# Kernel optimization log

Measured on AMD Instinct MI355X. Metric: run time of the kernel, lower is better.

## Reference

```python
import jax, jax.numpy as jnp
import numpy as np

DIM = 512
HEADS = 8
DHEAD = DIM // 8          # 64
INNER = HEADS * DHEAD     # 512
M_LANDMARKS = 256
PINV_ITERS = 6
KSZ = 33                  # residual depthwise conv kernel (default)


def setup_inputs() -> dict:
    key = jax.random.key(0)
    ks = jax.random.split(key, 5)
    B, N = 1, 16384
    s = DIM ** -0.5
    return {
        "x": jax.random.normal(ks[0], (B, N, DIM), jnp.float32),
        "norm_w": jnp.ones((DIM,), jnp.float32),
        "norm_b": jnp.zeros((DIM,), jnp.float32),
        "w_qkv": jax.random.normal(ks[1], (3 * INNER, DIM), jnp.float32) * s,   # Linear(dim, 3*inner, bias=False)
        "w_out": jax.random.normal(ks[2], (DIM, INNER), jnp.float32) * s,        # Linear(inner, dim)
        "b_out": jnp.zeros((DIM,), jnp.float32),
        "conv_w": jax.random.normal(ks[3], (HEADS, 1, KSZ, 1), jnp.float32) * 0.1,  # depthwise Conv2d(h,h,(33,1),groups=h)
    }


def _layernorm(x, w, b, eps=1e-5):
    mu = x.mean(-1, keepdims=True)
    var = ((x - mu) ** 2).mean(-1, keepdims=True)
    return (x - mu) * jax.lax.rsqrt(var + eps) * w + b


def _moore_penrose_pinv(a, iters):
    # a: [B, H, m, m]; matches lucidrains moore_penrose_iter_pinv (global max over col/row sums)
    abs_a = jnp.abs(a)
    col = abs_a.sum(-1).max()
    row = abs_a.sum(-2).max()
    z = jnp.swapaxes(a, -1, -2) / (col * row)
    I = jnp.eye(a.shape[-1], dtype=a.dtype)
    for _ in range(iters):
        az = a @ z
        z = 0.25 * z @ (13 * I - az @ (15 * I - az @ (7 * I - az)))
    return z


def _nystrom_attention(h, w_qkv, w_out, b_out, conv_w):
    B, N, _ = h.shape
    qkv = h @ w_qkv.T                          # [B, N, 3*inner]
    q, k, v = jnp.split(qkv, 3, axis=-1)

    def heads(t):
        return t.reshape(B, N, HEADS, DHEAD).transpose(0, 2, 1, 3)  # [B, H, N, d]
    q = heads(q) * (DHEAD ** -0.5)
    k = heads(k)
    v = heads(v)

    # landmark pooling: mean over contiguous groups of size l = N / m
    l = N // M_LANDMARKS
    q_l = q.reshape(B, HEADS, M_LANDMARKS, l, DHEAD).mean(3)   # [B, H, m, d]
    k_l = k.reshape(B, HEADS, M_LANDMARKS, l, DHEAD).mean(3)

    attn1 = jax.nn.softmax(jnp.einsum('bhnd,bhmd->bhnm', q, k_l), axis=-1)      # [B,H,N,m]
    attn2 = jax.nn.softmax(jnp.einsum('bhid,bhjd->bhij', q_l, k_l), axis=-1)    # [B,H,m,m]
    attn3 = jax.nn.softmax(jnp.einsum('bhmd,bhnd->bhmn', q_l, k), axis=-1)      # [B,H,m,N]

    attn2_inv = _moore_penrose_pinv(attn2, PINV_ITERS)
    out = attn1 @ (attn2_inv @ (attn3 @ v))                                     # [B,H,N,d]

    # residual depthwise conv along sequence dim (kernel 33x1, groups=HEADS, no bias)
    conv = jax.lax.conv_general_dilated(
        v, conv_w, window_strides=(1, 1),
        padding=((KSZ // 2, KSZ // 2), (0, 0)),
        dimension_numbers=('NCHW', 'OIHW', 'NCHW'),
        feature_group_count=HEADS)
    out = out + conv

    out = out.transpose(0, 2, 1, 3).reshape(B, N, INNER)
    return out @ w_out.T + b_out


def reference(x, norm_w, norm_b, w_qkv, w_out, b_out, conv_w):
    h = _layernorm(x, norm_w, norm_b)
    return x + _nystrom_attention(h, w_qkv, w_out, b_out, conv_w)
```

## Files before the change

kernel.cpp:

```cpp
#include <hip/hip_runtime.h>
#include <hip/hip_bf16.h>


typedef __attribute__((ext_vector_type(8))) short bf16x8;
typedef __attribute__((ext_vector_type(4))) float f32x4;

#define MFMA16(A, B, C) __builtin_amdgcn_mfma_f32_16x16x32_bf16(A, B, C, 0, 0, 0)
#define GLD16(g, l) __builtin_amdgcn_global_load_lds( \
    (const __attribute__((address_space(1))) void*)(g), \
    (__attribute__((address_space(3))) void*)(l), 16, 0, 0)

static __device__ __forceinline__ unsigned short f2b(float f) {
  __hip_bfloat16 h = __float2bfloat16(f);
  return *reinterpret_cast<unsigned short*>(&h);
}
static __device__ __forceinline__ float b2f(unsigned short u) {
  return __uint_as_float(((unsigned)u) << 16);
}

#define FMA16(ACC, AV, BV) do { \
  ACC[0][0] += AV.x*BV.x; ACC[0][1] += AV.x*BV.y; ACC[0][2] += AV.x*BV.z; ACC[0][3] += AV.x*BV.w; \
  ACC[1][0] += AV.y*BV.x; ACC[1][1] += AV.y*BV.y; ACC[1][2] += AV.y*BV.z; ACC[1][3] += AV.y*BV.w; \
  ACC[2][0] += AV.z*BV.x; ACC[2][1] += AV.z*BV.y; ACC[2][2] += AV.z*BV.z; ACC[2][3] += AV.z*BV.w; \
  ACC[3][0] += AV.w*BV.x; ACC[3][1] += AV.w*BV.y; ACC[3][2] += AV.w*BV.z; ACC[3][3] += AV.w*BV.w; \
} while (0)

__global__ __launch_bounds__(128) void k_ln(const float* __restrict__ x,
    const float* __restrict__ w, const float* __restrict__ b, unsigned short* __restrict__ h) {
  const int row = blockIdx.x;
  const int t = threadIdx.x;
  const float4 xv = ((const float4*)(x + (size_t)row * 512))[t];
  float s  = xv.x + xv.y + xv.z + xv.w;
  float sq = xv.x*xv.x + xv.y*xv.y + xv.z*xv.z + xv.w*xv.w;
  #pragma unroll
  for (int o = 32; o > 0; o >>= 1) {
    s  += __shfl_down(s, o, 64);
    sq += __shfl_down(sq, o, 64);
  }
  __shared__ float ls[2], lq[2];
  if ((t & 63) == 0) { ls[t >> 6] = s; lq[t >> 6] = sq; }
  __syncthreads();
  s = ls[0] + ls[1]; sq = lq[0] + lq[1];
  const float mean = s * (1.0f / 512.0f);
  const float var  = sq * (1.0f / 512.0f) - mean * mean;
  const float rstd = rsqrtf(var + 1e-5f);
  const float4 wv = ((const float4*)w)[t];
  const float4 bv = ((const float4*)b)[t];
  ushort4 hv;
  hv.x = f2b((xv.x - mean) * rstd * wv.x + bv.x);
  hv.y = f2b((xv.y - mean) * rstd * wv.y + bv.y);
  hv.z = f2b((xv.z - mean) * rstd * wv.z + bv.z);
  hv.w = f2b((xv.w - mean) * rstd * wv.w + bv.w);
  ((ushort4*)(h + (size_t)row * 512))[t] = hv;
}

__global__ __launch_bounds__(256) void k_cvt(const float* __restrict__ src,
    unsigned short* __restrict__ dst, int n4) {
  const int i = blockIdx.x * 256 + threadIdx.x;
  if (i < n4) {
    const float4 f = ((const float4*)src)[i];
    ushort4 u;
    u.x = f2b(f.x); u.y = f2b(f.y); u.z = f2b(f.z); u.w = f2b(f.w);
    ((ushort4*)dst)[i] = u;
  }
}

__global__ __launch_bounds__(256) void k_qkv_mfma(const unsigned short* __restrict__ A,
    const unsigned short* __restrict__ B,
    unsigned short* __restrict__ qb, unsigned short* __restrict__ kb,
    unsigned short* __restrict__ vb) {
  __shared__ unsigned short As[128 * 32];
  __shared__ unsigned short Bs[128 * 32];
  const int t = threadIdx.x;
  const int lane = t & 63, w = t >> 6;
  const int quad = lane >> 4, l15 = lane & 15;
  const int wm = (w >> 1) * 64, wn = (w & 1) * 64;
  const int m0 = blockIdx.y * 128, n0 = blockIdx.x * 128;
  f32x4 acc[4][4];
  #pragma unroll
  for (int i = 0; i < 4; ++i)
    #pragma unroll
    for (int j = 0; j < 4; ++j) acc[i][j] = (f32x4){0.f, 0.f, 0.f, 0.f};
  for (int k0 = 0; k0 < 512; k0 += 32) {
    __syncthreads();
    #pragma unroll
    for (int c = 0; c < 2; ++c) {
      const int slot = c * 256 + t;
      const int row = slot >> 2, seg = slot & 3;
      GLD16(A + (size_t)(m0 + row) * 512 + k0 + seg * 8, As + slot * 8);
      GLD16(B + (size_t)(n0 + row) * 512 + k0 + seg * 8, Bs + slot * 8);
    }
    __syncthreads();
    bf16x8 a[4], b[4];
    #pragma unroll
    for (int i = 0; i < 4; ++i)
      a[i] = *(const bf16x8*)(As + (wm + i * 16 + l15) * 32 + quad * 8);
    #pragma unroll
    for (int j = 0; j < 4; ++j)
      b[j] = *(const bf16x8*)(Bs + (wn + j * 16 + l15) * 32 + quad * 8);
    #pragma unroll
    for (int i = 0; i < 4; ++i)
      #pragma unroll
      for (int j = 0; j < 4; ++j)
        acc[i][j] = MFMA16(a[i], b[j], acc[i][j]);
  }
  const int part = n0 >> 9;
  #pragma unroll
  for (int i = 0; i < 4; ++i)
    #pragma unroll
    for (int j = 0; j < 4; ++j)
      #pragma unroll
      for (int r = 0; r < 4; ++r) {
        const int row = m0 + wm + i * 16 + quad * 4 + r;
        const int col = n0 + wn + j * 16 + l15;
        const int rem = col & 511;
        const int hd = rem >> 6, dd = rem & 63;
        const size_t idx = ((size_t)hd * 16384 + row) * 64 + dd;
        const float val = acc[i][j][r];
        if (part == 0)      qb[idx] = f2b(val * 0.125f);
        else if (part == 1) kb[idx] = f2b(val);
        else                vb[idx] = f2b(val);
      }
}

__global__ __launch_bounds__(256) void k_tr(const unsigned short* __restrict__ v,
    unsigned short* __restrict__ vt) {
  __shared__ unsigned short T[64][72];
  const int t = threadIdx.x;
  const int n0 = blockIdx.x * 64, h = blockIdx.y;
  const int n = t >> 2, sg = (t & 3) * 16;
  const unsigned short* p = v + ((size_t)(h * 16384 + n0 + n)) * 64 + sg;
  #pragma unroll
  for (int i = 0; i < 16; i += 4) {
    const ushort4 u = *(const ushort4*)(p + i);
    T[sg + i + 0][n] = u.x; T[sg + i + 1][n] = u.y;
    T[sg + i + 2][n] = u.z; T[sg + i + 3][n] = u.w;
  }
  __syncthreads();
  const int d = t >> 2, so = (t & 3) * 16;
  unsigned short* q = vt + ((size_t)(h * 64 + d)) * 16384 + n0 + so;
  #pragma unroll
  for (int i = 0; i < 16; i += 4) {
    ushort4 u;
    u.x = T[d][so + i]; u.y = T[d][so + i + 1];
    u.z = T[d][so + i + 2]; u.w = T[d][so + i + 3];
    *(ushort4*)(q + i) = u;
  }
}

__global__ __launch_bounds__(256) void k_landmark(const unsigned short* __restrict__ qb,
    const unsigned short* __restrict__ kb, float* __restrict__ qlf,
    unsigned short* __restrict__ qlb, float* __restrict__ klf,
    unsigned short* __restrict__ klb) {
  const int t = threadIdx.x, d = t & 63, grp = t >> 6;
  const int m = blockIdx.x, h = blockIdx.y;
  const unsigned short* src = blockIdx.z ? kb : qb;
  const unsigned short* p = src + ((size_t)h * 16384 + m * 64 + grp * 16) * 64 + d;
  float s = 0.f;
  #pragma unroll
  for (int i = 0; i < 16; ++i) s += b2f(p[(size_t)i * 64]);
  __shared__ float red[4][64];
  red[grp][d] = s;
  __syncthreads();
  if (t < 64) {
    float v = (red[0][d] + red[1][d]) + (red[2][d] + red[3][d]);
    v *= (1.0f / 64.0f);
    const size_t oi = ((size_t)h * 256 + m) * 64 + d;
    if (blockIdx.z == 0) { qlf[oi] = v; qlb[oi] = f2b(v); }
    else                 { klf[oi] = v; klb[oi] = f2b(v); }
  }
}

__global__ __launch_bounds__(256) void k_attn2(const float* __restrict__ ql,
    const float* __restrict__ kl, float* __restrict__ a2, unsigned short* __restrict__ a2b) {
  const int i = blockIdx.x, h = blockIdx.y, j = threadIdx.x;
  __shared__ float qrow[64];
  __shared__ float wred[4];
  __shared__ float wsum[4];
  if (j < 64) qrow[j] = ql[((size_t)h * 256 + i) * 64 + j];
  __syncthreads();
  const float* kr = kl + ((size_t)h * 256 + j) * 64;
  float s = 0.f;
  #pragma unroll 8
  for (int d = 0; d < 64; ++d) s += qrow[d] * kr[d];
  float mx = s;
  #pragma unroll
  for (int o2 = 32; o2 > 0; o2 >>= 1) mx = fmaxf(mx, __shfl_xor(mx, o2, 64));
  if ((j & 63) == 0) wred[j >> 6] = mx;
  __syncthreads();
  mx = fmaxf(fmaxf(wred[0], wred[1]), fmaxf(wred[2], wred[3]));
  const float e = __expf(s - mx);
  float sm = e;
  #pragma unroll
  for (int o2 = 32; o2 > 0; o2 >>= 1) sm += __shfl_xor(sm, o2, 64);
  if ((j & 63) == 0) wsum[j >> 6] = sm;
  __syncthreads();
  sm = wsum[0] + wsum[1] + wsum[2] + wsum[3];
  const float v = e / sm;
  const size_t idx = ((size_t)h * 256 + i) * 256 + j;
  a2[idx] = v;
  a2b[idx] = f2b(v);
}

__global__ __launch_bounds__(256) void k_colsum(const float* __restrict__ a2,
    float* __restrict__ cm) {
  const int h = blockIdx.x, j = threadIdx.x;
  const float* p = a2 + (size_t)h * 65536 + j;
  float s = 0.f;
  for (int i = 0; i < 256; ++i) s += p[(size_t)i * 256];
  float mx = s;
  #pragma unroll
  for (int o2 = 32; o2 > 0; o2 >>= 1) mx = fmaxf(mx, __shfl_xor(mx, o2, 64));
  __shared__ float wred[4];
  if ((j & 63) == 0) wred[j >> 6] = mx;
  __syncthreads();
  if (j == 0) cm[h] = fmaxf(fmaxf(wred[0], wred[1]), fmaxf(wred[2], wred[3]));
}

__global__ __launch_bounds__(256) void k_z0(const float* __restrict__ a2,
    const float* __restrict__ cm, unsigned short* __restrict__ z0b,
    unsigned short* __restrict__ z0t) {
  __shared__ float T[64][65];
  const int bi = blockIdx.x, bj = blockIdx.y, h = blockIdx.z;
  const int t = threadIdx.x;
  const int r = t >> 2, cseg = (t & 3) * 16;
  float g = cm[0];
  #pragma unroll
  for (int c = 1; c < 8; ++c) g = fmaxf(g, cm[c]);
  const float inv = 1.0f / g;
  const float* p = a2 + ((size_t)h * 256 + bj * 64 + r) * 256 + bi * 64 + cseg;
  unsigned short* qt = z0t + ((size_t)h * 256 + bj * 64 + r) * 256 + bi * 64 + cseg;
  #pragma unroll
  for (int i = 0; i < 16; i += 4) {
    const float4 f = *(const float4*)(p + i);
    T[cseg + i + 0][r] = f.x; T[cseg + i + 1][r] = f.y;
    T[cseg + i + 2][r] = f.z; T[cseg + i + 3][r] = f.w;
    ushort4 u;
    u.x = f2b(f.x * inv); u.y = f2b(f.y * inv);
    u.z = f2b(f.z * inv); u.w = f2b(f.w * inv);
    *(ushort4*)(qt + i) = u;
  }
  __syncthreads();
  unsigned short* qb_ = z0b + ((size_t)h * 256 + bi * 64 + r) * 256 + bj * 64 + cseg;
  #pragma unroll
  for (int i = 0; i < 16; i += 4) {
    ushort4 u;
    u.x = f2b(T[r][cseg + i] * inv);     u.y = f2b(T[r][cseg + i + 1] * inv);
    u.z = f2b(T[r][cseg + i + 2] * inv); u.w = f2b(T[r][cseg + i + 3] * inv);
    *(ushort4*)(qb_ + i) = u;
  }
}

__global__ __launch_bounds__(256) void k_pgemm(const unsigned short* __restrict__ A,
    const unsigned short* __restrict__ Bt, unsigned short* __restrict__ Cn,
    unsigned short* __restrict__ Ct, float* __restrict__ Cf,
    float alpha, float sdiag, int use_diag) {
  __shared__ unsigned short As[64 * 128];
  __shared__ unsigned short Bs[64 * 128];
  const int t = threadIdx.x;
  const int lane = t & 63, w = t >> 6;
  const int quad = lane >> 4, l15 = lane & 15;
  const int bn = blockIdx.x, bm = blockIdx.y, h = blockIdx.z;
  const size_t hs = (size_t)h * 65536;
  const unsigned short* Ap = A + hs + (size_t)(bm * 64) * 256;
  const unsigned short* Bp = Bt + hs + (size_t)(bn * 64) * 256;
  f32x4 acc[4];
  #pragma unroll
  for (int j = 0; j < 4; ++j) acc[j] = (f32x4){0.f, 0.f, 0.f, 0.f};
  for (int kh = 0; kh < 2; ++kh) {
    __syncthreads();
    #pragma unroll
    for (int c = 0; c < 4; ++c) {
      const int slot = c * 256 + t;
      const int row = slot >> 4, pc = slot & 15;
      const int lc = pc ^ (row & 7);
      GLD16(Ap + (size_t)row * 256 + kh * 128 + lc * 8, As + slot * 8);
      GLD16(Bp + (size_t)row * 256 + kh * 128 + lc * 8, Bs + slot * 8);
    }
    __syncthreads();
    #pragma unroll
    for (int kc = 0; kc < 4; ++kc) {
      const int arow = w * 16 + l15;
      const bf16x8 a = *(const bf16x8*)(As + arow * 128 + ((kc * 4 + quad) ^ (arow & 7)) * 8);
      #pragma unroll
      for (int j = 0; j < 4; ++j) {
        const int brow = j * 16 + l15;
        const bf16x8 b = *(const bf16x8*)(Bs + brow * 128 + ((kc * 4 + quad) ^ (brow & 7)) * 8);
        acc[j] = MFMA16(a, b, acc[j]);
      }
    }
  }
  const int row0 = bm * 64 + w * 16 + quad * 4;
  #pragma unroll
  for (int j = 0; j < 4; ++j) {
    const int col = bn * 64 + j * 16 + l15;
    float v[4];
    #pragma unroll
    for (int r = 0; r < 4; ++r) v[r] = acc[j][r] * alpha;
    if (Cn) {
      #pragma unroll
      for (int r = 0; r < 4; ++r) Cn[hs + (size_t)(row0 + r) * 256 + col] = f2b(v[r]);
    }
    if (Cf) {
      #pragma unroll
      for (int r = 0; r < 4; ++r) Cf[hs + (size_t)(row0 + r) * 256 + col] = v[r];
    }
    ushort4 u;
    float tv[4];
    #pragma unroll
    for (int r = 0; r < 4; ++r)
      tv[r] = use_diag ? ((col == row0 + r ? sdiag : 0.f) - v[r]) : v[r];
    u.x = f2b(tv[0]); u.y = f2b(tv[1]); u.z = f2b(tv[2]); u.w = f2b(tv[3]);
    *(ushort4*)(Ct + hs + (size_t)col * 256 + row0) = u;
  }
}

__global__ __launch_bounds__(256) void k_gemm256(const float* __restrict__ A,
    const float* __restrict__ B, float* __restrict__ C,
    int lda, int ldb, int ldc,
    unsigned long long sA, unsigned long long sB, unsigned long long sC,
    float alpha, float sdiag, int use_diag,
    const float* __restrict__ rs, unsigned long long sRS) {
  A += (size_t)blockIdx.z * sA;
  B += (size_t)blockIdx.z * sB;
  C += (size_t)blockIdx.z * sC;
  if (rs) rs += (size_t)blockIdx.z * sRS;
  __shared__ float As[16][68];
  __shared__ float Bs[16][68];
  const int t = threadIdx.x, tx = t & 15, ty = t >> 4;
  const int bn = blockIdx.x, bm = blockIdx.y;
  const int lr = t >> 2, lk = (t & 3) << 2;
  const int bkr = t >> 4, bnc = (t & 15) << 2;
  float acc[4][4] = {{0.f}};
  for (int k0 = 0; k0 < 256; k0 += 16) {
    float4 a4 = *(const float4*)(A + (size_t)(bm * 64 + lr) * lda + k0 + lk);
    float4 b4 = *(const float4*)(B + (size_t)(k0 + bkr) * ldb + bn * 64 + bnc);
    if (use_diag) {
      const int kg = k0 + bkr, ngb = bn * 64 + bnc;
      b4.x = (kg == ngb + 0 ? sdiag : 0.f) - b4.x;
      b4.y = (kg == ngb + 1 ? sdiag : 0.f) - b4.y;
      b4.z = (kg == ngb + 2 ? sdiag : 0.f) - b4.z;
      b4.w = (kg == ngb + 3 ? sdiag : 0.f) - b4.w;
    }
    if (rs) {
      const float rv = 1.0f / rs[k0 + bkr];
      b4.x *= rv; b4.y *= rv; b4.z *= rv; b4.w *= rv;
    }
    __syncthreads();
    As[lk+0][lr] = a4.x; As[lk+1][lr] = a4.y; As[lk+2][lr] = a4.z; As[lk+3][lr] = a4.w;
    *(float4*)&Bs[bkr][bnc] = b4;
    __syncthreads();
    #pragma unroll
    for (int kq = 0; kq < 16; ++kq) {
      const float4 av = *(const float4*)&As[kq][ty << 2];
      const float4 bv = *(const float4*)&Bs[kq][tx << 2];
      FMA16(acc, av, bv);
    }
  }
  #pragma unroll
  for (int ii = 0; ii < 4; ++ii)
    #pragma unroll
    for (int jj = 0; jj < 4; ++jj)
      C[(size_t)(bm * 64 + (ty << 2) + ii) * ldc + bn * 64 + (tx << 2) + jj] =
          alpha * acc[ii][jj];
}

__global__ __launch_bounds__(256) void k_trD(const float* __restrict__ D,
    unsigned short* __restrict__ dt) {
  __shared__ float T[64][65];
  const int t = threadIdx.x;
  const int mc = blockIdx.x, h = blockIdx.y;
  const int m = t >> 2, sg = (t & 3) * 16;
  const float* p = D + ((size_t)(h * 256 + mc * 64 + m)) * 64 + sg;
  #pragma unroll
  for (int i = 0; i < 16; i += 4) {
    const float4 f = *(const float4*)(p + i);
    T[sg + i + 0][m] = f.x; T[sg + i + 1][m] = f.y;
    T[sg + i + 2][m] = f.z; T[sg + i + 3][m] = f.w;
  }
  __syncthreads();
  const int d = t >> 2, so = (t & 3) * 16;
  unsigned short* q = dt + ((size_t)(h * 64 + d)) * 256 + mc * 64 + so;
  #pragma unroll
  for (int i = 0; i < 16; i += 4) {
    ushort4 u;
    u.x = f2b(T[d][so + i]);     u.y = f2b(T[d][so + i + 1]);
    u.z = f2b(T[d][so + i + 2]); u.w = f2b(T[d][so + i + 3]);
    *(ushort4*)(q + i) = u;
  }
}

__global__ __launch_bounds__(256) void k_w3_mfma(const unsigned short* __restrict__ qlb,
    const unsigned short* __restrict__ kb, const unsigned short* __restrict__ vt,
    float* __restrict__ W, float* __restrict__ lsum) {
  __shared__ unsigned short QLs[64 * 64];
  __shared__ unsigned short Ks [64 * 64];
  __shared__ unsigned short Vts[64 * 64];
  __shared__ unsigned short Ps [64 * 64];
  const int t = threadIdx.x;
  const int lane = t & 63, w = t >> 6;
  const int quad = lane >> 4, l15 = lane & 15;
  const int kc = blockIdx.x, mt = blockIdx.y, h = blockIdx.z;
  #pragma unroll
  for (int c = 0; c < 2; ++c) {
    const int slot = c * 256 + t;
    const int row = slot >> 3, pc = slot & 7, lc = pc ^ (row & 7);
    GLD16(qlb + ((size_t)(h * 256 + mt * 64 + row)) * 64 + lc * 8, QLs + slot * 8);
  }
  __syncthreads();
  const int arow = w * 16 + l15;
  const bf16x8 aq0 = *(const bf16x8*)(QLs + arow * 64 + ((quad    ) ^ (arow & 7)) * 8);
  const bf16x8 aq1 = *(const bf16x8*)(QLs + arow * 64 + ((quad + 4) ^ (arow & 7)) * 8);
  f32x4 wacc[4];
  #pragma unroll
  for (int dt = 0; dt < 4; ++dt) wacc[dt] = (f32x4){0.f, 0.f, 0.f, 0.f};
  float lacc[4] = {0.f, 0.f, 0.f, 0.f};
  for (int ss = 0; ss < 16; ++ss) {
    const int n0 = kc * 1024 + ss * 64;
    __syncthreads();
    #pragma unroll
    for (int c = 0; c < 2; ++c) {
      const int slot = c * 256 + t;
      const int row = slot >> 3, pc = slot & 7, lc = pc ^ (row & 7);
      GLD16(kb + ((size_t)(h * 16384 + n0 + row)) * 64 + lc * 8, Ks + slot * 8);
      GLD16(vt + ((size_t)(h * 64 + row)) * 16384 + n0 + lc * 8, Vts + slot * 8);
    }
    __syncthreads();
    f32x4 s[4];
    #pragma unroll
    for (int j = 0; j < 4; ++j) {
      s[j] = (f32x4){0.f, 0.f, 0.f, 0.f};
      const int brow = j * 16 + l15;
      const bf16x8 b0 = *(const bf16x8*)(Ks + brow * 64 + ((quad    ) ^ (brow & 7)) * 8);
      const bf16x8 b1 = *(const bf16x8*)(Ks + brow * 64 + ((quad + 4) ^ (brow & 7)) * 8);
      s[j] = MFMA16(aq0, b0, s[j]);
      s[j] = MFMA16(aq1, b1, s[j]);
    }
    #pragma unroll
    for (int j = 0; j < 4; ++j)
      #pragma unroll
      for (int r = 0; r < 4; ++r) {
        const float e = __expf(s[j][r]);
        lacc[r] += e;
        const int prow = w * 16 + quad * 4 + r, pcol = j * 16 + l15;
        Ps[prow * 64 + (((pcol >> 3) ^ (prow & 7)) << 3) + (pcol & 7)] = f2b(e);
      }
    __syncthreads();
    const bf16x8 ap0 = *(const bf16x8*)(Ps + arow * 64 + ((quad    ) ^ (arow & 7)) * 8);
    const bf16x8 ap1 = *(const bf16x8*)(Ps + arow * 64 + ((quad + 4) ^ (arow & 7)) * 8);
    #pragma unroll
    for (int dt = 0; dt < 4; ++dt) {
      const int brow = dt * 16 + l15;
      const bf16x8 b0 = *(const bf16x8*)(Vts + brow * 64 + ((quad    ) ^ (brow & 7)) * 8);
      const bf16x8 b1 = *(const bf16x8*)(Vts + brow * 64 + ((quad + 4) ^ (brow & 7)) * 8);
      wacc[dt] = MFMA16(ap0, b0, wacc[dt]);
      wacc[dt] = MFMA16(ap1, b1, wacc[dt]);
    }
  }
  #pragma unroll
  for (int dt = 0; dt < 4; ++dt)
    #pragma unroll
    for (int r = 0; r < 4; ++r)
      atomicAdd(&W[((size_t)(h * 256 + mt * 64 + w * 16 + quad * 4 + r)) * 64 + dt * 16 + l15],
                wacc[dt][r]);
  #pragma unroll
  for (int r = 0; r < 4; ++r) {
    #pragma unroll
    for (int msk = 1; msk < 16; msk <<= 1) lacc[r] += __shfl_xor(lacc[r], msk, 64);
    if (l15 == 0)
      atomicAdd(&lsum[h * 256 + mt * 64 + w * 16 + quad * 4 + r], lacc[r]);
  }
}
// ... 28 lines not shown
    const int n = t >> 2;
    const int gb = (t & 3) * 24;
    #pragma unroll
    for (int i = 0; i < 24; ++i) {
      const int g = gb + i;
      const int j = g - n;
      const int src = n0 - 16 + g;
      const float val = (j >= 0 && j <= 32 && src >= 0 && src < 16384) ? Wsm[j] : 0.f;
      Wb[n * 96 + (((g >> 3) ^ (n & 3)) << 3) + (g & 7)] = f2b(val);
    }
  }
  __syncthreads();
  f32x4 cacc[4];
  #pragma unroll
  for (int dt = 0; dt < 4; ++dt) cacc[dt] = (f32x4){0.f, 0.f, 0.f, 0.f};
  #pragma unroll
  for (int kcc = 0; kcc < 3; ++kcc) {
    const bf16x8 a = *(const bf16x8*)(Wb + arow * 96 + (((kcc * 4 + quad) ^ (arow & 3)) << 3));
    int off = n0 - 16 + kcc * 32 + quad * 8;
    off = off < 0 ? 0 : (off > 16376 ? 16376 : off);
    #pragma unroll
    for (int dt = 0; dt < 4; ++dt) {
      const bf16x8 b = *(const bf16x8*)(vt + ((size_t)(h * 64 + dt * 16 + l15)) * 16384 + off);
      cacc[dt] = MFMA16(a, b, cacc[dt]);
    }
  }
  f32x4 oacc[4];
  #pragma unroll
  for (int dt = 0; dt < 4; ++dt) oacc[dt] = (f32x4){0.f, 0.f, 0.f, 0.f};
  float lacc[4] = {0.f, 0.f, 0.f, 0.f};
  for (int mc = 0; mc < 4; ++mc) {
    const int m0 = mc * 64;
    __syncthreads();
    #pragma unroll
    for (int c = 0; c < 2; ++c) {
      const int slot = c * 256 + t;
      const int row = slot >> 3, pc = slot & 7, lc = pc ^ (row & 7);
      GLD16(klb + ((size_t)(h * 256 + m0 + row)) * 64 + lc * 8, Ks + slot * 8);
      GLD16(dtb + ((size_t)(h * 64 + row)) * 256 + m0 + lc * 8, Ds + slot * 8);
    }
    __syncthreads();
    f32x4 s[4];
    #pragma unroll
    for (int j = 0; j < 4; ++j) {
      s[j] = (f32x4){0.f, 0.f, 0.f, 0.f};
      const int brow = j * 16 + l15;
      const bf16x8 b0 = *(const bf16x8*)(Ks + brow * 64 + ((quad    ) ^ (brow & 7)) * 8);
      const bf16x8 b1 = *(const bf16x8*)(Ks + brow * 64 + ((quad + 4) ^ (brow & 7)) * 8);
      s[j] = MFMA16(aq0, b0, s[j]);
      s[j] = MFMA16(aq1, b1, s[j]);
    }
    #pragma unroll
    for (int j = 0; j < 4; ++j)
      #pragma unroll
      for (int r = 0; r < 4; ++r) {
        const float e = __expf(s[j][r]);
        lacc[r] += e;
        const int prow = w * 16 + quad * 4 + r, pcol = j * 16 + l15;
        Ps[prow * 64 + (((pcol >> 3) ^ (prow & 7)) << 3) + (pcol & 7)] = f2b(e);
      }
    __syncthreads();
    const bf16x8 ap0 = *(const bf16x8*)(Ps + arow * 64 + ((quad    ) ^ (arow & 7)) * 8);
    const bf16x8 ap1 = *(const bf16x8*)(Ps + arow * 64 + ((quad + 4) ^ (arow & 7)) * 8);
    #pragma unroll
    for (int dt = 0; dt < 4; ++dt) {
      const int brow = dt * 16 + l15;
      const bf16x8 b0 = *(const bf16x8*)(Ds + brow * 64 + ((quad    ) ^ (brow & 7)) * 8);
      const bf16x8 b1 = *(const bf16x8*)(Ds + brow * 64 + ((quad + 4) ^ (brow & 7)) * 8);
      oacc[dt] = MFMA16(ap0, b0, oacc[dt]);
      oacc[dt] = MFMA16(ap1, b1, oacc[dt]);
    }
  }
  #pragma unroll
  for (int r = 0; r < 4; ++r)
    #pragma unroll
    for (int msk = 1; msk < 16; msk <<= 1) lacc[r] += __shfl_xor(lacc[r], msk, 64);
  #pragma unroll
  for (int dt = 0; dt < 4; ++dt)
    #pragma unroll
    for (int r = 0; r < 4; ++r) {
      const float val = oacc[dt][r] / lacc[r] + cacc[dt][r];
      o[((size_t)(n0 + w * 16 + quad * 4 + r)) * 512 + h * 64 + dt * 16 + l15] = f2b(val);
    }
}

__global__ __launch_bounds__(256) void k_out_mfma(const unsigned short* __restrict__ A,
    const unsigned short* __restrict__ B, const float* __restrict__ bias,
    const float* __restrict__ xres, float* __restrict__ out) {
  __shared__ unsigned short As[128 * 32];
  __shared__ unsigned short Bs[128 * 32];
  const int t = threadIdx.x;
  const int lane = t & 63, w = t >> 6;
  const int quad = lane >> 4, l15 = lane & 15;
  const int wm = (w >> 1) * 64, wn = (w & 1) * 64;
  const int m0 = blockIdx.y * 128, n0 = blockIdx.x * 128;
  f32x4 acc[4][4];
  #pragma unroll
  for (int i = 0; i < 4; ++i)
    #pragma unroll
    for (int j = 0; j < 4; ++j) acc[i][j] = (f32x4){0.f, 0.f, 0.f, 0.f};
  for (int k0 = 0; k0 < 512; k0 += 32) {
    __syncthreads();
    #pragma unroll
    for (int c = 0; c < 2; ++c) {
      const int slot = c * 256 + t;
      const int row = slot >> 2, seg = slot & 3;
      GLD16(A + (size_t)(m0 + row) * 512 + k0 + seg * 8, As + slot * 8);
      GLD16(B + (size_t)(n0 + row) * 512 + k0 + seg * 8, Bs + slot * 8);
    }
    __syncthreads();
    bf16x8 a[4], b[4];
    #pragma unroll
    for (int i = 0; i < 4; ++i)
      a[i] = *(const bf16x8*)(As + (wm + i * 16 + l15) * 32 + quad * 8);
    #pragma unroll
    for (int j = 0; j < 4; ++j)
      b[j] = *(const bf16x8*)(Bs + (wn + j * 16 + l15) * 32 + quad * 8);
    #pragma unroll
    for (int i = 0; i < 4; ++i)
      #pragma unroll
      for (int j = 0; j < 4; ++j)
        acc[i][j] = MFMA16(a[i], b[j], acc[i][j]);
  }
  #pragma unroll
  for (int i = 0; i < 4; ++i)
    #pragma unroll
    for (int j = 0; j < 4; ++j)
      #pragma unroll
      for (int r = 0; r < 4; ++r) {
        const int row = m0 + wm + i * 16 + quad * 4 + r;
        const int col = n0 + wn + j * 16 + l15;
        out[(size_t)row * 512 + col] = acc[i][j][r] + bias[col] + xres[(size_t)row * 512 + col];
      }
}

extern "C" void kernel_launch(void* const* d_in, const int* in_sizes, int n_in,
                              void* d_out, int out_size, void* d_ws, size_t ws_size,
                              hipStream_t stream) {
  const float* x      = (const float*)d_in[0];
  const float* norm_w = (const float*)d_in[1];
  const float* norm_b = (const float*)d_in[2];
  const float* w_qkv  = (const float*)d_in[3];
  const float* w_out  = (const float*)d_in[4];
  const float* b_out  = (const float*)d_in[5];
  const float* conv_w = (const float*)d_in[6];
  float* out = (float*)d_out;

  char* cur = (char*)d_ws;
  auto alloc = [&](size_t bytes) -> char* {
    char* p = cur;
    cur += (bytes + 255) & ~(size_t)255;
    return p;
  };
  const size_t NB = (size_t)16384 * 512;
  const size_t LM = (size_t)8 * 256 * 64;
  const size_t SQ = (size_t)8 * 256 * 256;

  unsigned short* h_b  = (unsigned short*)alloc(NB * 2);
  unsigned short* wq_b = (unsigned short*)alloc((size_t)1536 * 512 * 2);
  unsigned short* wo_b = (unsigned short*)alloc((size_t)512 * 512 * 2);
  unsigned short* qb   = (unsigned short*)alloc(NB * 2);
  unsigned short* kb   = (unsigned short*)alloc(NB * 2);
  unsigned short* vb   = (unsigned short*)alloc(NB * 2);
  unsigned short* vt   = (unsigned short*)alloc(NB * 2);
  float*          qlf  = (float*)alloc(LM * 4);
  float*          klf  = (float*)alloc(LM * 4);
  unsigned short* qlb  = (unsigned short*)alloc(LM * 2);
  unsigned short* klb  = (unsigned short*)alloc(LM * 2);
  float*          a2   = (float*)alloc(SQ * 4);
  unsigned short* a2b  = (unsigned short*)alloc(SQ * 2);
  unsigned short* z0b  = (unsigned short*)alloc(SQ * 2);
  unsigned short* z0t  = (unsigned short*)alloc(SQ * 2);
  unsigned short* Pn   = (unsigned short*)alloc(SQ * 2);
  unsigned short* Pt   = (unsigned short*)alloc(SQ * 2);
  unsigned short* Q1t  = (unsigned short*)alloc(SQ * 2);
  unsigned short* Q2t  = (unsigned short*)alloc(SQ * 2);
  unsigned short* zp0n = (unsigned short*)alloc(SQ * 2);
  unsigned short* zp0t = (unsigned short*)alloc(SQ * 2);
  unsigned short* zp1n = (unsigned short*)alloc(SQ * 2);
  unsigned short* zp1t = (unsigned short*)alloc(SQ * 2);
  float*          zf5  = (float*)alloc(SQ * 4);
  float*          zfin = (float*)alloc(SQ * 4);
  float*          Pp   = (float*)alloc(SQ * 4);
  float*          Q1   = (float*)alloc(SQ * 4);
  float*          Q2   = (float*)alloc(SQ * 4);
  float*          W    = (float*)alloc(LM * 4 + 2048 * 4);
  float*          lsum = W + LM;
  float*          D    = (float*)alloc(LM * 4);
  unsigned short* dtb  = (unsigned short*)alloc(LM * 2);
  float*          cm   = (float*)alloc(64 * 4);
  unsigned short* o_b  = (unsigned short*)alloc(NB * 2);

  hipMemsetAsync(W, 0, (LM + 2048) * sizeof(float), stream);
  k_ln<<<16384, 128, 0, stream>>>(x, norm_w, norm_b, h_b);
  k_cvt<<<768, 256, 0, stream>>>(w_qkv, wq_b, 196608);
  k_cvt<<<256, 256, 0, stream>>>(w_out, wo_b, 65536);
  k_qkv_mfma<<<dim3(12, 128), 256, 0, stream>>>(h_b, wq_b, qb, kb, vb);
  k_tr<<<dim3(256, 8), 256, 0, stream>>>(vb, vt);
  k_landmark<<<dim3(256, 8, 2), 256, 0, stream>>>(qb, kb, qlf, qlb, klf, klb);
  k_attn2<<<dim3(256, 8), 256, 0, stream>>>(qlf, klf, a2, a2b);
  k_colsum<<<8, 256, 0, stream>>>(a2, cm);
  k_z0<<<dim3(4, 4, 8), 256, 0, stream>>>(a2, cm, z0b, z0t);

  unsigned short* zan = z0b; unsigned short* zat = z0t;
  for (int it = 0; it < 5; ++it) {
    unsigned short* zbn = (it & 1) ? zp1n : zp0n;
    unsigned short* zbt = (it & 1) ? zp1t : zp0t;
    k_pgemm<<<dim3(4, 4, 8), 256, 0, stream>>>(a2b, zat, Pn, Pt, nullptr, 1.f, 7.f, 1);
    k_pgemm<<<dim3(4, 4, 8), 256, 0, stream>>>(Pn, Pt, nullptr, Q1t, nullptr, 1.f, 15.f, 1);
    k_pgemm<<<dim3(4, 4, 8), 256, 0, stream>>>(Pn, Q1t, nullptr, Q2t, nullptr, 1.f, 13.f, 1);
    k_pgemm<<<dim3(4, 4, 8), 256, 0, stream>>>(zan, Q2t, zbn, zbt,
        it == 4 ? zf5 : nullptr, 0.25f, 0.f, 0);
    zan = zbn; zat = zbt;
  }
  k_gemm256<<<dim3(4, 4, 8), 256, 0, stream>>>(a2, zf5, Pp, 256, 256, 256,
      65536ULL, 65536ULL, 65536ULL, 1.f, 0.f, 0, nullptr, 0ULL);
  k_gemm256<<<dim3(4, 4, 8), 256, 0, stream>>>(Pp, Pp, Q1, 256, 256, 256,
      65536ULL, 65536ULL, 65536ULL, 1.f, 7.f, 1, nullptr, 0ULL);
  k_gemm256<<<dim3(4, 4, 8), 256, 0, stream>>>(Pp, Q1, Q2, 256, 256, 256,
      65536ULL, 65536ULL, 65536ULL, 1.f, 15.f, 1, nullptr, 0ULL);
  k_gemm256<<<dim3(4, 4, 8), 256, 0, stream>>>(zf5, Q2, zfin, 256, 256, 256,
      65536ULL, 65536ULL, 65536ULL, 0.25f, 13.f, 1, nullptr, 0ULL);

  k_w3_mfma<<<dim3(16, 4, 8), 256, 0, stream>>>(qlb, kb, vt, W, lsum);
  k_gemm256<<<dim3(1, 4, 8), 256, 0, stream>>>(zfin, W, D, 256, 64, 64,
      65536ULL, 16384ULL, 16384ULL, 1.f, 0.f, 0, lsum, 256ULL);
  k_trD<<<dim3(4, 8), 256, 0, stream>>>(D, dtb);
  k_attn1_mfma<<<dim3(256, 8), 256, 0, stream>>>(qb, klb, dtb, vt, conv_w, o_b);
  k_out_mfma<<<dim3(4, 128), 256, 0, stream>>>(o_b, wo_b, b_out, x, out);
}
```

Baseline: 449.1 us.

## Rewrite QKV and output GEMMs with 256x256 tiles and triple-buffered LDS pipeline

Replaces the 128x128 single-buffered QKV and output-projection GEMMs with 512-thread 256x256 tile kernels. Global-to-LDS loads are triple-buffered using vmcnt waits and a single barrier per k-step, and MFMA issue is raised in priority with s_setprio. Block indices are swizzled for L2 locality. The fragment-friendly LDS layout removes bank conflicts. The larger tiles cut operand reloads, but the output GEMM now runs only 128 blocks, which may underfill the GPU's CUs, and 96KB of LDS per block limits occupancy.

```diff
diff --git a/kernel.cpp b/kernel.cpp
--- a/kernel.cpp
+++ b/kernel.cpp
@@ -65,62 +65,128 @@
   }
 }
 
-__global__ __launch_bounds__(256) void k_qkv_mfma(const unsigned short* __restrict__ A,
+__device__ __forceinline__ void stage_tile(const unsigned short* __restrict__ A,
+    const unsigned short* __restrict__ B, unsigned short* lds,
+    int m0, int n0, int k0, int tid) {
+  #pragma unroll
+  for (int c = 0; c < 2; ++c) {
+    const int s = c * 512 + tid;
+    const int grow = ((s >> 6) << 4) | (s & 15);
+    const int chunk = (s >> 4) & 3;
+    GLD16(A + (size_t)(m0 + grow) * 512 + k0 + chunk * 8, lds + s * 8);
+    GLD16(B + (size_t)(n0 + grow) * 512 + k0 + chunk * 8, lds + 8192 + s * 8);
+  }
+}
+
+__device__ __forceinline__ void compute_tile(const unsigned short* lds,
+    f32x4 (&acc)[8][4], int wr, int wc, int quad, int l15) {
+  bf16x8 a[8], b[4];
+  #pragma unroll
+  for (int i = 0; i < 8; ++i)
+    a[i] = *(const bf16x8*)(lds + (size_t)((wr * 8 + i) * 64 + quad * 16 + l15) * 8);
+  #pragma unroll
+  for (int j = 0; j < 4; ++j)
+    b[j] = *(const bf16x8*)(lds + 8192 + (size_t)((wc * 4 + j) * 64 + quad * 16 + l15) * 8);
+  __builtin_amdgcn_s_setprio(1);
+  #pragma unroll
+  for (int i = 0; i < 8; ++i)
+    #pragma unroll
+    for (int j = 0; j < 4; ++j)
+      acc[i][j] = MFMA16(a[i], b[j], acc[i][j]);
+  __builtin_amdgcn_s_setprio(0);
+}
+
+#define GEMM256_PIPELINE(Aptr, Bptr, M0, N0)                                 \
+  f32x4 acc[8][4];                                                           \
+  _Pragma("unroll")                                                          \
+  for (int i = 0; i < 8; ++i)                                                \
+    _Pragma("unroll")                                                        \
+    for (int j = 0; j < 4; ++j) acc[i][j] = (f32x4){0.f, 0.f, 0.f, 0.f};     \
+  stage_tile(Aptr, Bptr, lds, M0, N0, 0, tid);                               \
+  asm volatile("" ::: "memory");                                             \
+  stage_tile(Aptr, Bptr, lds + 16384, M0, N0, 32, tid);                      \
+  asm volatile("s_waitcnt vmcnt(4)" ::: "memory");                           \
+  __builtin_amdgcn_s_barrier();                                              \
+  {                                                                          \
+    int cb = 0, sb = 2;                                                      \
+    for (int t = 0; t < 14; ++t) {                                           \
+      stage_tile(Aptr, Bptr, lds + sb * 16384, M0, N0, (t + 2) * 32, tid);   \
+      compute_tile(lds + cb * 16384, acc, wr, wc, quad, l15);                \
+      asm volatile("s_waitcnt vmcnt(4)" ::: "memory");                       \
+      __builtin_amdgcn_s_barrier();                                          \
+      cb = (cb == 2) ? 0 : cb + 1;                                           \
+      sb = (sb == 2) ? 0 : sb + 1;                                           \
+    }                                                                        \
+    compute_tile(lds + cb * 16384, acc, wr, wc, quad, l15);                  \
+    cb = (cb == 2) ? 0 : cb + 1;                                             \
+    asm volatile("s_waitcnt vmcnt(0)" ::: "memory");                         \
+    __builtin_amdgcn_s_barrier();                                            \
+    compute_tile(lds + cb * 16384, acc, wr, wc, quad, l15);                  \
+  }
+
+__global__ __launch_bounds__(512, 2) void k_qkv2(const unsigned short* __restrict__ A,
     const unsigned short* __restrict__ B,
     unsigned short* __restrict__ qb, unsigned short* __restrict__ kb,
     unsigned short* __restrict__ vb) {
-  __shared__ unsigned short As[128 * 32];
-  __shared__ unsigned short Bs[128 * 32];
-  const int t = threadIdx.x;
-  const int lane = t & 63, w = t >> 6;
+  __shared__ unsigned short lds[49152];
+  const int tid = threadIdx.x;
+  const int lane = tid & 63, w = tid >> 6;
+  const int wr = w >> 2, wc = w & 3;
   const int quad = lane >> 4, l15 = lane & 15;
-  const int wm = (w >> 1) * 64, wn = (w & 1) * 64;
-  const int m0 = blockIdx.y * 128, n0 = blockIdx.x * 128;
-  f32x4 acc[4][4];
-  #pragma unroll
-  for (int i = 0; i < 4; ++i)
-    #pragma unroll
-    for (int j = 0; j < 4; ++j) acc[i][j] = (f32x4){0.f, 0.f, 0.f, 0.f};
-  for (int k0 = 0; k0 < 512; k0 += 32) {
-    __syncthreads();
-    #pragma unroll
-    for (int c = 0; c < 2; ++c) {
-      const int slot = c * 256 + t;
-      const int row = slot >> 2, seg = slot & 3;
-      GLD16(A + (size_t)(m0 + row) * 512 + k0 + seg * 8, As + slot * 8);
-      GLD16(B + (size_t)(n0 + row) * 512 + k0 + seg * 8, Bs + slot * 8);
-    }
-    __syncthreads();
-    bf16x8 a[4], b[4];
-    #pragma unroll
-    for (int i = 0; i < 4; ++i)
-      a[i] = *(const bf16x8*)(As + (wm + i * 16 + l15) * 32 + quad * 8);
-    #pragma unroll
-    for (int j = 0; j < 4; ++j)
-      b[j] = *(const bf16x8*)(Bs + (wn + j * 16 + l15) * 32 + quad * 8);
-    #pragma unroll
-    for (int i = 0; i < 4; ++i)
+  const int bid = blockIdx.x;
+  const int swz = (bid & 7) * 48 + (bid >> 3);
+  const int by = swz / 6, bx = swz - by * 6;
+  const int m0 = by * 256, n0 = bx * 256;
+
+  GEMM256_PIPELINE(A, B, m0, n0)
+
+  const int part = n0 >> 9;
+  const int head = ((n0 & 511) >> 6) + wc;
+  unsigned short* dst = (part == 0) ? qb : (part == 1) ? kb : vb;
+  const float scale = (part == 0) ? 0.125f : 1.0f;
+  unsigned short* dp = dst + (size_t)head * 16384 * 64;
+  #pragma unroll
+  for (int i = 0; i < 8; ++i) {
+    const int rowb = m0 + wr * 128 + i * 16 + quad * 4;
+    #pragma unroll
+    for (int j = 0; j < 4; ++j) {
+      const int dd = j * 16 + l15;
       #pragma unroll
-      for (int j = 0; j < 4; ++j)
-        acc[i][j] = MFMA16(a[i], b[j], acc[i][j]);
-  }
-  const int part = n0 >> 9;
-  #pragma unroll
-  for (int i = 0; i < 4; ++i)
-    #pragma unroll
-    for (int j = 0; j < 4; ++j)
+      for (int r = 0; r < 4; ++r)
+        dp[(size_t)(rowb + r) * 64 + dd] = f2b(acc[i][j][r] * scale);
+    }
+  }
+}
+
+__global__ __launch_bounds__(512, 2) void k_out2(const unsigned short* __restrict__ A,
+    const unsigned short* __restrict__ B, const float* __restrict__ bias,
+    const float* __restrict__ xres, float* __restrict__ out) {
+  __shared__ unsigned short lds[49152];
+  const int tid = threadIdx.x;
+  const int lane = tid & 63, w = tid >> 6;
+  const int wr = w >> 2, wc = w & 3;
+  const int quad = lane >> 4, l15 = lane & 15;
+  const int bid = blockIdx.x;
+  const int swz = (bid & 7) * 16 + (bid >> 3);
+  const int by = swz >> 1, bx = swz & 1;
+  const int m0 = by * 256, n0 = bx * 256;
+
+  GEMM256_PIPELINE(A, B, m0, n0)
+
+  #pragma unroll
+  for (int j = 0; j < 4; ++j) {
+    const int col = n0 + wc * 64 + j * 16 + l15;
+    const float bv = bias[col];
+    #pragma unroll
+    for (int i = 0; i < 8; ++i) {
+      const int rowb = m0 + wr * 128 + i * 16 + quad * 4;
       #pragma unroll
       for (int r = 0; r < 4; ++r) {
-        const int row = m0 + wm + i * 16 + quad * 4 + r;
-        const int col = n0 + wn + j * 16 + l15;
-        const int rem = col & 511;
-        const int hd = rem >> 6, dd = rem & 63;
-        const size_t idx = ((size_t)hd * 16384 + row) * 64 + dd;
-        const float val = acc[i][j][r];
-        if (part == 0)      qb[idx] = f2b(val * 0.125f);
-        else if (part == 1) kb[idx] = f2b(val);
-        else                vb[idx] = f2b(val);
+        const size_t idx = (size_t)(rowb + r) * 512 + col;
+        out[idx] = acc[i][j][r] + bv + xres[idx];
       }
+    }
+  }
 }
 
 __global__ __launch_bounds__(256) void k_tr(const unsigned short* __restrict__ v,
@@ -582,56 +648,6 @@
       const float val = oacc[dt][r] / lacc[r] + cacc[dt][r];
       o[((size_t)(n0 + w * 16 + quad * 4 + r)) * 512 + h * 64 + dt * 16 + l15] = f2b(val);
     }
-}
-
-__global__ __launch_bounds__(256) void k_out_mfma(const unsigned short* __restrict__ A,
-    const unsigned short* __restrict__ B, const float* __restrict__ bias,
-    const float* __restrict__ xres, float* __restrict__ out) {
-  __shared__ unsigned short As[128 * 32];
-  __shared__ unsigned short Bs[128 * 32];
-  const int t = threadIdx.x;
-  const int lane = t & 63, w = t >> 6;
-  const int quad = lane >> 4, l15 = lane & 15;
-  const int wm = (w >> 1) * 64, wn = (w & 1) * 64;
-  const int m0 = blockIdx.y * 128, n0 = blockIdx.x * 128;
-  f32x4 acc[4][4];
-  #pragma unroll
-  for (int i = 0; i < 4; ++i)
-    #pragma unroll
-    for (int j = 0; j < 4; ++j) acc[i][j] = (f32x4){0.f, 0.f, 0.f, 0.f};
-  for (int k0 = 0; k0 < 512; k0 += 32) {
-    __syncthreads();
-    #pragma unroll
-    for (int c = 0; c < 2; ++c) {
-      const int slot = c * 256 + t;
-      const int row = slot >> 2, seg = slot & 3;
-      GLD16(A + (size_t)(m0 + row) * 512 + k0 + seg * 8, As + slot * 8);
-      GLD16(B + (size_t)(n0 + row) * 512 + k0 + seg * 8, Bs + slot * 8);
-    }
-    __syncthreads();
-    bf16x8 a[4], b[4];
-    #pragma unroll
-    for (int i = 0; i < 4; ++i)
-      a[i] = *(const bf16x8*)(As + (wm + i * 16 + l15) * 32 + quad * 8);
-    #pragma unroll
-    for (int j = 0; j < 4; ++j)
-      b[j] = *(const bf16x8*)(Bs + (wn + j * 16 + l15) * 32 + quad * 8);
-    #pragma unroll
-    for (int i = 0; i < 4; ++i)
-      #pragma unroll
-      for (int j = 0; j < 4; ++j)
-        acc[i][j] = MFMA16(a[i], b[j], acc[i][j]);
-  }
-  #pragma unroll
-  for (int i = 0; i < 4; ++i)
-    #pragma unroll
-    for (int j = 0; j < 4; ++j)
-      #pragma unroll
-      for (int r = 0; r < 4; ++r) {
-        const int row = m0 + wm + i * 16 + quad * 4 + r;
-        const int col = n0 + wn + j * 16 + l15;
-        out[(size_t)row * 512 + col] = acc[i][j][r] + bias[col] + xres[(size_t)row * 512 + col];
-      }
 }
 
 extern "C" void kernel_launch(void* const* d_in, const int* in_sizes, int n_in,
@@ -695,7 +711,7 @@
   k_ln<<<16384, 128, 0, stream>>>(x, norm_w, norm_b, h_b);
   k_cvt<<<768, 256, 0, stream>>>(w_qkv, wq_b, 196608);
   k_cvt<<<256, 256, 0, stream>>>(w_out, wo_b, 65536);
-  k_qkv_mfma<<<dim3(12, 128), 256, 0, stream>>>(h_b, wq_b, qb, kb, vb);
+  k_qkv2<<<384, 512, 0, stream>>>(h_b, wq_b, qb, kb, vb);
   k_tr<<<dim3(256, 8), 256, 0, stream>>>(vb, vt);
   k_landmark<<<dim3(256, 8, 2), 256, 0, stream>>>(qb, kb, qlf, qlb, klf, klb);
   k_attn2<<<dim3(256, 8), 256, 0, stream>>>(qlf, klf, a2, a2b);
@@ -727,5 +743,5 @@
       65536ULL, 16384ULL, 16384ULL, 1.f, 0.f, 0, lsum, 256ULL);
   k_trD<<<dim3(4, 8), 256, 0, stream>>>(D, dtb);
   k_attn1_mfma<<<dim3(256, 8), 256, 0, stream>>>(qb, klb, dtb, vt, conv_w, o_b);
-  k_out_mfma<<<dim3(4, 128), 256, 0, stream>>>(o_b, wo_b, b_out, x, out);
-}
+  k_out2<<<128, 512, 0, stream>>>(o_b, wo_b, b_out, x, out);
+}
```

Measured after the change: 464.1 us. +3.3%, slower.

## Fuse pinv iterations into one persistent per-head kernel and fold D transpose

Applied to the files above, without the earlier changes.

Replaces the 20 separate small bf16 GEMM launches of the first five pseudo-inverse iterations with one kernel that runs one 512-thread block per head. Each block computes full 256x256 products with double-buffered LDS staging and block barriers between steps. The transpose of D is fused into a new GEMM kernel that applies the row-sum normalisation and writes bf16 transposed output directly. The W3 kernel is moved earlier in the stream. This removes launch overhead and inter-kernel gaps, but uses only 8 blocks for the pinv work, so most of the GPU sits idle during that phase.

```diff
diff --git a/kernel.cpp b/kernel.cpp
--- a/kernel.cpp
+++ b/kernel.cpp
@@ -251,67 +251,132 @@
   }
 }
 
-__global__ __launch_bounds__(256) void k_pgemm(const unsigned short* __restrict__ A,
-    const unsigned short* __restrict__ Bt, unsigned short* __restrict__ Cn,
-    unsigned short* __restrict__ Ct, float* __restrict__ Cf,
-    float alpha, float sdiag, int use_diag) {
-  __shared__ unsigned short As[64 * 128];
-  __shared__ unsigned short Bs[64 * 128];
-  const int t = threadIdx.x;
-  const int lane = t & 63, w = t >> 6;
+__device__ __forceinline__ void pv_gemm(const unsigned short* __restrict__ Ah,
+    const unsigned short* __restrict__ Bh,
+    unsigned short* __restrict__ Cn, unsigned short* __restrict__ Ct,
+    float* __restrict__ Cf, float alpha, float sdiag, int use_diag,
+    unsigned short (&As)[2][8192], unsigned short (&Bs)[2][8192],
+    int tid, int wr, int wc, int quad, int l15) {
+  f32x4 acc[8][4];
+  #pragma unroll
+  for (int i = 0; i < 8; ++i)
+    #pragma unroll
+    for (int j = 0; j < 4; ++j) acc[i][j] = (f32x4){0.f, 0.f, 0.f, 0.f};
+
+#define PV_STAGE(buf, k0) do { \
+    _Pragma("unroll") \
+    for (int c = 0; c < 2; ++c) { \
+      const int s_ = c * 512 + tid; \
+      const int row_ = ((s_ >> 6) << 4) | (s_ & 15); \
+      const int ch_ = (s_ >> 4) & 3; \
+      GLD16(Ah + (size_t)row_ * 256 + (k0) + ch_ * 8, &As[buf][s_ * 8]); \
+      GLD16(Bh + (size_t)row_ * 256 + (k0) + ch_ * 8, &Bs[buf][s_ * 8]); \
+    } \
+  } while (0)
+
+#define PV_COMP(buf) do { \
+    bf16x8 a_[8], b_[4]; \
+    _Pragma("unroll") \
+    for (int i = 0; i < 8; ++i) \
+      a_[i] = *(const bf16x8*)(&As[buf][((wr * 8 + i) * 64 + quad * 16 + l15) * 8]); \
+    _Pragma("unroll") \
+    for (int j = 0; j < 4; ++j) \
+      b_[j] = *(const bf16x8*)(&Bs[buf][((wc * 4 + j) * 64 + quad * 16 + l15) * 8]); \
+    __builtin_amdgcn_s_setprio(1); \
+    _Pragma("unroll") \
+    for (int i = 0; i < 8; ++i) \
+      _Pragma("unroll") \
+      for (int j = 0; j < 4; ++j) \
+        acc[i][j] = MFMA16(a_[i], b_[j], acc[i][j]); \
+    __builtin_amdgcn_s_setprio(0); \
+  } while (0)
+
+  PV_STAGE(0, 0);
+  asm volatile("" ::: "memory");
+  PV_STAGE(1, 32);
+  asm volatile("s_waitcnt vmcnt(4)" ::: "memory");
+  __builtin_amdgcn_s_barrier();
+  #pragma unroll 1
+  for (int t = 0; t < 6; ++t) {
+    PV_COMP(t & 1);
+    asm volatile("" ::: "memory");
+    __builtin_amdgcn_s_barrier();
+    asm volatile("" ::: "memory");
+    PV_STAGE(t & 1, (t + 2) * 32);
+    asm volatile("s_waitcnt vmcnt(4)" ::: "memory");
+    __builtin_amdgcn_s_barrier();
+  }
+  PV_COMP(0);
+  asm volatile("s_waitcnt vmcnt(0)" ::: "memory");
+  __builtin_amdgcn_s_barrier();
+  PV_COMP(1);
+#undef PV_STAGE
+#undef PV_COMP
+
+  #pragma unroll
+  for (int i = 0; i < 8; ++i) {
+    const int row0 = wr * 128 + i * 16 + quad * 4;
+    #pragma unroll
+    for (int j = 0; j < 4; ++j) {
+      const int col = wc * 64 + j * 16 + l15;
+      float v[4];
+      #pragma unroll
+      for (int r = 0; r < 4; ++r) v[r] = acc[i][j][r] * alpha;
+      if (Cn) {
+        #pragma unroll
+        for (int r = 0; r < 4; ++r) Cn[(size_t)(row0 + r) * 256 + col] = f2b(v[r]);
+      }
+      if (Cf) {
+        #pragma unroll
+        for (int r = 0; r < 4; ++r) Cf[(size_t)(row0 + r) * 256 + col] = v[r];
+      }
+      float tv[4];
+      #pragma unroll
+      for (int r = 0; r < 4; ++r)
+        tv[r] = use_diag ? ((col == row0 + r ? sdiag : 0.f) - v[r]) : v[r];
+      ushort4 u;
+      u.x = f2b(tv[0]); u.y = f2b(tv[1]); u.z = f2b(tv[2]); u.w = f2b(tv[3]);
+      *(ushort4*)(Ct + (size_t)col * 256 + row0) = u;
+    }
+  }
+}
+
+__global__ __launch_bounds__(512) void k_pinv5(
+    const unsigned short* __restrict__ a2b,
+    const unsigned short* __restrict__ z0b, const unsigned short* __restrict__ z0t,
+    unsigned short* __restrict__ zp0n, unsigned short* __restrict__ zp0t,
+    unsigned short* __restrict__ zp1n, unsigned short* __restrict__ zp1t,
+    unsigned short* __restrict__ Pn, unsigned short* __restrict__ Pt,
+    unsigned short* __restrict__ Q1t, unsigned short* __restrict__ Q2t,
+    float* __restrict__ zf5) {
+  __shared__ __align__(16) unsigned short As[2][8192];
+  __shared__ __align__(16) unsigned short Bs[2][8192];
+  const int tid = threadIdx.x;
+  const int lane = tid & 63, w = tid >> 6;
+  const int wr = w >> 2, wc = w & 3;
   const int quad = lane >> 4, l15 = lane & 15;
-  const int bn = blockIdx.x, bm = blockIdx.y, h = blockIdx.z;
-  const size_t hs = (size_t)h * 65536;
-  const unsigned short* Ap = A + hs + (size_t)(bm * 64) * 256;
-  const unsigned short* Bp = Bt + hs + (size_t)(bn * 64) * 256;
-  f32x4 acc[4];
-  #pragma unroll
-  for (int j = 0; j < 4; ++j) acc[j] = (f32x4){0.f, 0.f, 0.f, 0.f};
-  for (int kh = 0; kh < 2; ++kh) {
-    __syncthreads();
-    #pragma unroll
-    for (int c = 0; c < 4; ++c) {
-      const int slot = c * 256 + t;
-      const int row = slot >> 4, pc = slot & 15;
-      const int lc = pc ^ (row & 7);
-      GLD16(Ap + (size_t)row * 256 + kh * 128 + lc * 8, As + slot * 8);
-      GLD16(Bp + (size_t)row * 256 + kh * 128 + lc * 8, Bs + slot * 8);
-    }
-    __syncthreads();
-    #pragma unroll
-    for (int kc = 0; kc < 4; ++kc) {
-      const int arow = w * 16 + l15;
-      const bf16x8 a = *(const bf16x8*)(As + arow * 128 + ((kc * 4 + quad) ^ (arow & 7)) * 8);
-      #pragma unroll
-      for (int j = 0; j < 4; ++j) {
-        const int brow = j * 16 + l15;
-        const bf16x8 b = *(const bf16x8*)(Bs + brow * 128 + ((kc * 4 + quad) ^ (brow & 7)) * 8);
-        acc[j] = MFMA16(a, b, acc[j]);
-      }
-    }
-  }
-  const int row0 = bm * 64 + w * 16 + quad * 4;
-  #pragma unroll
-  for (int j = 0; j < 4; ++j) {
-    const int col = bn * 64 + j * 16 + l15;
-    float v[4];
-    #pragma unroll
-    for (int r = 0; r < 4; ++r) v[r] = acc[j][r] * alpha;
-    if (Cn) {
-      #pragma unroll
-      for (int r = 0; r < 4; ++r) Cn[hs + (size_t)(row0 + r) * 256 + col] = f2b(v[r]);
-    }
-    if (Cf) {
-      #pragma unroll
-      for (int r = 0; r < 4; ++r) Cf[hs + (size_t)(row0 + r) * 256 + col] = v[r];
-    }
-    ushort4 u;
-    float tv[4];
-    #pragma unroll
-    for (int r = 0; r < 4; ++r)
-      tv[r] = use_diag ? ((col == row0 + r ? sdiag : 0.f) - v[r]) : v[r];
-    u.x = f2b(tv[0]); u.y = f2b(tv[1]); u.z = f2b(tv[2]); u.w = f2b(tv[3]);
-    *(ushort4*)(Ct + hs + (size_t)col * 256 + row0) = u;
+  const size_t hs = (size_t)blockIdx.x * 65536;
+  const unsigned short* a2h = a2b + hs;
+  unsigned short* PnH = Pn + hs;
+  unsigned short* PtH = Pt + hs;
+  unsigned short* Q1H = Q1t + hs;
+  unsigned short* Q2H = Q2t + hs;
+  const unsigned short* zan = z0b + hs;
+  const unsigned short* zat = z0t + hs;
+  #pragma unroll 1
+  for (int it = 0; it < 5; ++it) {
+    unsigned short* zbn = ((it & 1) ? zp1n : zp0n) + hs;
+    unsigned short* zbt = ((it & 1) ? zp1t : zp0t) + hs;
+    pv_gemm(a2h, zat, PnH, PtH, nullptr, 1.f, 7.f, 1, As, Bs, tid, wr, wc, quad, l15);
+    __syncthreads();
+    pv_gemm(PnH, PtH, nullptr, Q1H, nullptr, 1.f, 15.f, 1, As, Bs, tid, wr, wc, quad, l15);
+    __syncthreads();
+    pv_gemm(PnH, Q1H, nullptr, Q2H, nullptr, 1.f, 13.f, 1, As, Bs, tid, wr, wc, quad, l15);
+    __syncthreads();
+    pv_gemm(zan, Q2H, zbn, zbt, (it == 4) ? (zf5 + hs) : nullptr, 0.25f, 0.f, 0,
+            As, Bs, tid, wr, wc, quad, l15);
+    __syncthreads();
+    zan = zbn; zat = zbt;
   }
 }
 
@@ -365,29 +430,42 @@
           alpha * acc[ii][jj];
 }
 
-__global__ __launch_bounds__(256) void k_trD(const float* __restrict__ D,
-    unsigned short* __restrict__ dt) {
-  __shared__ float T[64][65];
-  const int t = threadIdx.x;
-  const int mc = blockIdx.x, h = blockIdx.y;
-  const int m = t >> 2, sg = (t & 3) * 16;
-  const float* p = D + ((size_t)(h * 256 + mc * 64 + m)) * 64 + sg;
-  #pragma unroll
-  for (int i = 0; i < 16; i += 4) {
-    const float4 f = *(const float4*)(p + i);
-    T[sg + i + 0][m] = f.x; T[sg + i + 1][m] = f.y;
-    T[sg + i + 2][m] = f.z; T[sg + i + 3][m] = f.w;
-  }
-  __syncthreads();
-  const int d = t >> 2, so = (t & 3) * 16;
-  unsigned short* q = dt + ((size_t)(h * 64 + d)) * 256 + mc * 64 + so;
-  #pragma unroll
-  for (int i = 0; i < 16; i += 4) {
-    ushort4 u;
-    u.x = f2b(T[d][so + i]);     u.y = f2b(T[d][so + i + 1]);
-    u.z = f2b(T[d][so + i + 2]); u.w = f2b(T[d][so + i + 3]);
-    *(ushort4*)(q + i) = u;
-  }
+__global__ __launch_bounds__(256) void k_gemmD(const float* __restrict__ A,
+    const float* __restrict__ B, const float* __restrict__ rs,
+    unsigned short* __restrict__ dtb) {
+  __shared__ float Asf[16 * 68];
+  __shared__ float Bsf[16 * 68];
+  const int bm = blockIdx.x, h = blockIdx.y;
+  A += (size_t)h * 65536;
+  B += (size_t)h * 16384;
+  rs += (size_t)h * 256;
+  const int t = threadIdx.x, tx = t & 15, ty = t >> 4;
+  const int lr = t >> 2, lk = (t & 3) << 2;
+  const int bkr = t >> 4, bnc = (t & 15) << 2;
+  float acc[4][4] = {{0.f}};
+  for (int k0 = 0; k0 < 256; k0 += 16) {
+    float4 a4 = *(const float4*)(A + (size_t)(bm * 64 + lr) * 256 + k0 + lk);
+    float4 b4 = *(const float4*)(B + (size_t)(k0 + bkr) * 64 + bnc);
+    const float rv = 1.0f / rs[k0 + bkr];
+    b4.x *= rv; b4.y *= rv; b4.z *= rv; b4.w *= rv;
+    __syncthreads();
+    Asf[(lk + 0) * 68 + lr] = a4.x; Asf[(lk + 1) * 68 + lr] = a4.y;
+    Asf[(lk + 2) * 68 + lr] = a4.z; Asf[(lk + 3) * 68 + lr] = a4.w;
+    *(float4*)&Bsf[bkr * 68 + bnc] = b4;
+    __syncthreads();
+    #pragma unroll
+    for (int kq = 0; kq < 16; ++kq) {
+      const float4 av = *(const float4*)&Asf[kq * 68 + (ty << 2)];
+      const float4 bv = *(const float4*)&Bsf[kq * 68 + (tx << 2)];
+      FMA16(acc, av, bv);
+    }
+  }
+  #pragma unroll
+  for (int ii = 0; ii < 4; ++ii)
+    #pragma unroll
+    for (int jj = 0; jj < 4; ++jj)
+      dtb[(size_t)(h * 64 + (tx << 2) + jj) * 256 + bm * 64 + (ty << 2) + ii] =
+          f2b(acc[ii][jj]);
 }
 
 __global__ __launch_bounds__(256) void k_w3_mfma(const unsigned short* __restrict__ qlb,
@@ -686,7 +764,6 @@
   float*          Q2   = (float*)alloc(SQ * 4);
   float*          W    = (float*)alloc(LM * 4 + 2048 * 4);
   float*          lsum = W + LM;
-  float*          D    = (float*)alloc(LM * 4);
   unsigned short* dtb  = (unsigned short*)alloc(LM * 2);
   float*          cm   = (float*)alloc(64 * 4);
   unsigned short* o_b  = (unsigned short*)alloc(NB * 2);
@@ -701,18 +778,11 @@
   k_attn2<<<dim3(256, 8), 256, 0, stream>>>(qlf, klf, a2, a2b);
   k_colsum<<<8, 256, 0, stream>>>(a2, cm);
   k_z0<<<dim3(4, 4, 8), 256, 0, stream>>>(a2, cm, z0b, z0t);
-
-  unsigned short* zan = z0b; unsigned short* zat = z0t;
-  for (int it = 0; it < 5; ++it) {
-    unsigned short* zbn = (it & 1) ? zp1n : zp0n;
-    unsigned short* zbt = (it & 1) ? zp1t : zp0t;
-    k_pgemm<<<dim3(4, 4, 8), 256, 0, stream>>>(a2b, zat, Pn, Pt, nullptr, 1.f, 7.f, 1);
-    k_pgemm<<<dim3(4, 4, 8), 256, 0, stream>>>(Pn, Pt, nullptr, Q1t, nullptr, 1.f, 15.f, 1);
-    k_pgemm<<<dim3(4, 4, 8), 256, 0, stream>>>(Pn, Q1t, nullptr, Q2t, nullptr, 1.f, 13.f, 1);
-    k_pgemm<<<dim3(4, 4, 8), 256, 0, stream>>>(zan, Q2t, zbn, zbt,
-        it == 4 ? zf5 : nullptr, 0.25f, 0.f, 0);
-    zan = zbn; zat = zbt;
-  }
+  k_w3_mfma<<<dim3(16, 4, 8), 256, 0, stream>>>(qlb, kb, vt, W, lsum);
+
+  k_pinv5<<<8, 512, 0, stream>>>(a2b, z0b, z0t, zp0n, zp0t, zp1n, zp1t,
+                                 Pn, Pt, Q1t, Q2t, zf5);
+
   k_gemm256<<<dim3(4, 4, 8), 256, 0, stream>>>(a2, zf5, Pp, 256, 256, 256,
       65536ULL, 65536ULL, 65536ULL, 1.f, 0.f, 0, nullptr, 0ULL);
   k_gemm256<<<dim3(4, 4, 8), 256, 0, stream>>>(Pp, Pp, Q1, 256, 256, 256,
@@ -722,10 +792,8 @@
   k_gemm256<<<dim3(4, 4, 8), 256, 0, stream>>>(zf5, Q2, zfin, 256, 256, 256,
       65536ULL, 65536ULL, 65536ULL, 0.25f, 13.f, 1, nullptr, 0ULL);
 
-  k_w3_mfma<<<dim3(16, 4, 8), 256, 0, stream>>>(qlb, kb, vt, W, lsum);
-  k_gemm256<<<dim3(1, 4, 8), 256, 0, stream>>>(zfin, W, D, 256, 64, 64,
-      65536ULL, 16384ULL, 16384ULL, 1.f, 0.f, 0, lsum, 256ULL);
-  k_trD<<<dim3(4, 8), 256, 0, stream>>>(D, dtb);
+  k_gemmD<<<dim3(4, 8), 256, 0, stream>>>(zfin, W, lsum, dtb);
+
   k_attn1_mfma<<<dim3(256, 8), 256, 0, stream>>>(qb, klb, dtb, vt, conv_w, o_b);
   k_out_mfma<<<dim3(4, 128), 256, 0, stream>>>(o_b, wo_b, b_out, x, out);
 }
```

Result: slower. 872.8 us (+94.3%).
